# Kernel optimization log

Hardware: AMD Instinct MI355X
Metric: run time of the kernel (lower is better)

Reference implementation:

```python
import jax, jax.numpy as jnp
import numpy as np

# ----- static layer configuration (mirrors __init__ / _precompute_cg_tensor) -----
NODE_LS = [0, 0, 1, 1]          # node_l_values (multiplicity expressed via repetition; node_multiplicity=1)
EDGE_SH = 1                      # edge_sh_degree
H_LS = NODE_LS + NODE_LS + [0]   # l-values of h = [f_src, f_tgt, d]
H_DIMS = [2 * l + 1 for l in H_LS]
H_OFF = np.concatenate([[0], np.cumsum(H_DIMS)])
A_DIMS = [2 * l + 1 for l in range(EDGE_SH + 1)]
A_OFF = np.concatenate([[0], np.cumsum(A_DIMS)])
O_DIMS = [2 * l + 1 for l in NODE_LS]
O_OFF = np.concatenate([[0], np.cumsum(O_DIMS)])
F_DIM = int(O_OFF[-1])           # 8
A_DIM = int(A_OFF[-1])           # 4
N_NODES, N_EDGES = 100000, 1600000
MLP_DIMS = [2 * len(NODE_LS) + 1, 64, 32, len(NODE_LS)]  # 9 -> 64 -> 32 -> 4

def _levi_civita():
    e = np.zeros((3, 3, 3), np.float32)
    e[0, 1, 2] = e[1, 2, 0] = e[2, 0, 1] = 1.0
    e[0, 2, 1] = e[2, 1, 0] = e[1, 0, 2] = -1.0
    return e

# real SO(3) Clebsch-Gordan tensors (e3nn wigner_3j normalization: full contraction norm 1)
_CG = {
    (0, 0, 0): np.ones((1, 1, 1), np.float32),
    (0, 1, 1): (np.eye(3, dtype=np.float32) / np.sqrt(3.0)).reshape(1, 3, 3),
    (1, 0, 1): (np.eye(3, dtype=np.float32) / np.sqrt(3.0)).reshape(3, 1, 3),
    (1, 1, 0): (np.eye(3, dtype=np.float32) / np.sqrt(3.0)).reshape(3, 3, 1),
    (1, 1, 1): _levi_civita() / np.sqrt(6.0),
}

CONNECTIONS = []  # (h_idx, a_l, out_idx, cg[h,a,o]) -- same enumeration order as the torch loop
for _h_idx, _hl in enumerate(H_LS):
    for _al in range(EDGE_SH + 1):
        for _oi, _ol in enumerate(NODE_LS):
            if abs(_hl - _al) <= _ol <= _hl + _al and (_hl, _al, _ol) in _CG:
                CONNECTIONS.append((_h_idx, _al, _oi, jnp.asarray(_CG[(_hl, _al, _ol)])))


def _invariants(x):
    # s_i = [f_{l=0}, ||f_{l=1}||, ...] per l-slot (multiplicity 1)
    outs = []
    for i, l in enumerate(NODE_LS):
        s, e = int(O_OFF[i]), int(O_OFF[i + 1])
        if l == 0:
            outs.append(x[:, s:e])
        else:
            outs.append(jnp.linalg.norm(x[:, s:e], axis=1, keepdims=True))
    return jnp.concatenate(outs, axis=1)


def setup_inputs() -> dict:
    ks = jax.random.split(jax.random.key(0), 10)
    edge_index = jax.random.randint(ks[0], (2, N_EDGES), 0, N_NODES)
    f = jax.random.normal(ks[1], (N_NODES, F_DIM), jnp.float32)
    d = jax.random.uniform(ks[2], (N_EDGES, 1), jnp.float32)
    a = jax.random.normal(ks[3], (N_EDGES, A_DIM), jnp.float32)
    w1 = jax.random.normal(ks[4], (EDGE_SH + 1,), jnp.float32) * 0.1
    w2 = jax.random.normal(ks[5], (EDGE_SH + 1,), jnp.float32) * 0.1
    W0 = jax.random.normal(ks[6], (MLP_DIMS[0], MLP_DIMS[1]), jnp.float32) / np.sqrt(MLP_DIMS[0])
    b0 = jnp.zeros((MLP_DIMS[1],), jnp.float32)
    W1 = jax.random.normal(ks[7], (MLP_DIMS[1], MLP_DIMS[2]), jnp.float32) / np.sqrt(MLP_DIMS[1])
    b1 = jnp.zeros((MLP_DIMS[2],), jnp.float32)
    W2 = jax.random.normal(ks[8], (MLP_DIMS[2], MLP_DIMS[3]), jnp.float32) / np.sqrt(MLP_DIMS[2])
    b2 = jnp.zeros((MLP_DIMS[3],), jnp.float32)
    return {"edge_index": edge_index, "f": f, "d": d, "a": a, "w1": w1, "w2": w2,
            "W0": W0, "b0": b0, "W1": W1, "b1": b1, "W2": W2, "b2": b2}


def reference(edge_index, f, d, a, w1, w2, W0, b0, W1, b1, W2, b2):
    src, tgt = edge_index[0], edge_index[1]
    n = f.shape[0]
    h = jnp.concatenate([f[src], f[tgt], d], axis=1)  # [E, 17]
    messages = jnp.zeros((h.shape[0], F_DIM), f.dtype)
    for h_idx, a_l, out_idx, cg in CONNECTIONS:
        hs, he = int(H_OFF[h_idx]), int(H_OFF[h_idx + 1])
        as_, ae = int(A_OFF[a_l]), int(A_OFF[a_l + 1])
        os_, oe = int(O_OFF[out_idx]), int(O_OFF[out_idx + 1])
        raw = jnp.einsum('hao,eh,ea->eo', cg, h[:, hs:he], a[:, as_:ae])  # [E, 2*out_l+1]
        msg = jnp.tanh(w2[a_l] * jnp.tanh(w1[a_l] * raw))
        messages = messages.at[:, os_:oe].add(msg)
    agg = jax.ops.segment_sum(messages, tgt, num_segments=n)          # [N, 8]
    dist_sum = jax.ops.segment_sum(d, tgt, num_segments=n)           # [N, 1]
    counts = jax.ops.segment_sum(jnp.ones((h.shape[0],), f.dtype), tgt, num_segments=n)
    avg_d = dist_sum / (counts[:, None] + 1e-8)
    psi_in = jnp.concatenate([_invariants(f), _invariants(agg), avg_d], axis=1)  # [N, 9]
    x = jax.nn.relu(psi_in @ W0 + b0)
    x = jax.nn.relu(x @ W1 + b1)
    gates = jax.nn.sigmoid(x @ W2 + b2)  # [N, 4]
    gate_full = jnp.concatenate(
        [jnp.repeat(gates[:, i:i + 1], O_DIMS[i], axis=1) for i in range(len(NODE_LS))], axis=1)
    return f + gate_full * agg
```

## Files before the change

kernel.cpp:

```cpp
#include <hip/hip_runtime.h>
#include <math.h>

#define IS3 0.57735026918962576f
#define IS6 0.40824829046386302f

#define SHIFT 11
#define BSZ   2048
#define CAP   36864u
#define MQ    4096.0f
#define IMQ   (1.0f/4096.0f)

typedef float v2f __attribute__((ext_vector_type(2)));

__device__ __forceinline__ float fastrcp(float x) { return __builtin_amdgcn_rcpf(x); }
__device__ __forceinline__ v2f mk2(float a, float b) { v2f r; r.x = a; r.y = b; return r; }

__device__ __forceinline__ v2f Tnl2(v2f x, v2f tw1, v2f w2) {
    v2f t = tw1 * x;
    v2f e;
    e.x = __expf(t.x);
    e.y = __expf(t.y);
    v2f ep = e + 1.0f;
    v2f r;
    r.x = fastrcp(ep.x);
    r.y = fastrcp(ep.y);
    v2f u = 1.0f - 2.0f * r;
    v2f z = w2 * u;
    v2f z2 = z * z;
    v2f p = z2 * 0.133333333f - 0.333333333f;
    return z * z2 * p + z;
}

__device__ __forceinline__ int q16(float x) {
    int v = (int)rintf(x * MQ);
    v = v >  32767 ?  32767 : v;
    v = v < -32768 ? -32768 : v;
    return v;
}

__global__ __launch_bounds__(256, 8) void route_kernel(
    const int* __restrict__ ei, const float* __restrict__ f,
    const float* __restrict__ d, const float* __restrict__ a,
    const float* __restrict__ w1p, const float* __restrict__ w2p,
    unsigned* __restrict__ tails,
    unsigned* __restrict__ qmeta,
    uint2* __restrict__ qmsg,
    int E, int nbuk)
{
    __shared__ unsigned hcnt[64];
    __shared__ unsigned hoff[64];
    int tid = threadIdx.x;
    if (tid < 64) hcnt[tid] = 0;

    int e = blockIdx.x * 256 + tid;
    bool valid = (e < E);

    float tw10 = 2.0f * w1p[0], tw11 = 2.0f * w1p[1];
    float w20 = w2p[0], w21 = w2p[1];

    int t = 0, s = 0;
    float4 sA = make_float4(0.f,0.f,0.f,0.f), sB = sA, tA = sA, tB = sA, av = sA;
    float de = 0.f;
    if (valid) {
        t = ei[E + e];
        s = ei[e];
        const float4* f4 = (const float4*)f;
        sA = f4[2*s]; sB = f4[2*s+1];
        tA = f4[2*t]; tB = f4[2*t+1];
        de = d[e];
        av = ((const float4*)a)[e];
    }

    __syncthreads();

    unsigned b = 0, lrank = 0;
    if (valid) {
        b = (((unsigned)t) >> SHIFT) & 63u;
        lrank = atomicAdd(&hcnt[b], 1u);
    }
    __syncthreads();

    unsigned basek = 0;
    if (tid < nbuk && hcnt[tid] != 0u)
        basek = atomicAdd(&tails[tid * 64], hcnt[tid]);

    unsigned dq = 0;
    uint2 pk = make_uint2(0u, 0u);
    if (valid) {
        float a0 = av.x, ax = av.y, ay = av.z, az = av.w;
        float axs = ax * IS3, ays = ay * IS3, azs = az * IS3;
        float a03 = a0 * IS3;

        v2f twSX = mk2(tw10, tw11), w2SX = mk2(w20, w21);
        v2f twXY = mk2(tw11, tw11), w2XY = mk2(w21, w21);
        v2f twCX = mk2(tw11, tw10), w2CX = mk2(w21, w20);
        v2f twDD = mk2(tw10, tw10), w2DD = mk2(w20, w20);

        v2f aSX = mk2(a0, axs);
        v2f aYZ = mk2(ays, azs);

        float sc[5] = { sA.x, sA.y, tA.x, tA.y, de };
        float vx[4] = { sA.z, sB.y, tA.z, tB.y };
        float vy[4] = { sA.w, sB.z, tA.w, tB.z };
        float vz[4] = { sB.x, sB.w, tB.x, tB.w };

        v2f mSX = mk2(0.f, 0.f);
        v2f mYZ = mk2(0.f, 0.f);
        float cz6[4];

        #pragma unroll
        for (int i = 0; i < 5; ++i) {
            mSX += Tnl2(sc[i] * aSX, twSX, w2SX);
            mYZ += Tnl2(sc[i] * aYZ, twXY, w2XY);
        }
        #pragma unroll
        for (int i = 0; i < 4; ++i) {
            float dva = vx[i]*ax + vy[i]*ay + vz[i]*az;
            mSX += Tnl2(mk2(dva * IS3, vx[i] * a03), twCX, w2CX);
            mYZ += Tnl2(mk2(vy[i] * a03, vz[i] * a03), twDD, w2DD);
            float cx = vy[i]*az - vz[i]*ay;
            float cy = vz[i]*ax - vx[i]*az;
            float cz = vx[i]*ay - vy[i]*ax;
            v2f exy = Tnl2(mk2(cx * IS6, cy * IS6), twXY, w2XY);
            mSX.y += exy.x;
            mYZ.x += exy.y;
            cz6[i] = cz * IS6;
        }
        v2f g1 = Tnl2(mk2(cz6[0], cz6[1]), twXY, w2XY);
        v2f g2 = Tnl2(mk2(cz6[2], cz6[3]), twXY, w2XY);
        mYZ.y += (g1.x + g1.y) + (g2.x + g2.y);

        unsigned dqi = (unsigned)(de * 2047.0f + 0.5f);
        dq = dqi > 2047u ? 2047u : dqi;
        int qS = q16(mSX.x), qX = q16(mSX.y), qY = q16(mYZ.x), qZ = q16(mYZ.y);
        pk.x = ((unsigned)(unsigned short)qS) | (((unsigned)(unsigned short)qX) << 16);
        pk.y = ((unsigned)(unsigned short)qY) | (((unsigned)(unsigned short)qZ) << 16);
    }

    if (tid < nbuk) hoff[tid] = basek;
    __syncthreads();

    if (valid) {
        unsigned pos = hoff[b] + lrank;
        if (pos < CAP) {
            size_t idx = (size_t)b * CAP + pos;
            qmeta[idx] = (((unsigned)(t & (BSZ - 1))) << 11) | dq;
            qmsg[idx]  = pk;
        }
    }
}

__global__ __launch_bounds__(1024) void bucket_kernel(
    const unsigned* __restrict__ tails, const unsigned* __restrict__ qmeta,
    const uint2* __restrict__ qmsg, unsigned* __restrict__ partial,
    int nbuk, int seg)
{
    __shared__ unsigned long long accSX[BSZ];
    __shared__ unsigned long long accYZ[BSZ];
    __shared__ unsigned accM[BSZ];
    int wg = blockIdx.x;
    int b = wg / seg, sgi = wg % seg;
    for (int i = threadIdx.x; i < BSZ; i += 1024) {
        accSX[i] = 0ull; accYZ[i] = 0ull; accM[i] = 0u;
    }
    __syncthreads();

    unsigned tail = tails[b * 64];
    if (tail > CAP) tail = CAP;
    unsigned lo = (unsigned)(((unsigned long long)tail * sgi) / seg);
    unsigned hi = (unsigned)(((unsigned long long)tail * (sgi + 1)) / seg);
    size_t base = (size_t)b * CAP;

    for (unsigned q = lo + threadIdx.x; q < hi; q += 1024) {
        unsigned meta = qmeta[base + q];
        uint2 m = qmsg[base + q];
        int local = (int)(meta >> 11);
        int qS = (int)(short)(m.x & 0xFFFFu);
        int qX = (int)(short)(m.x >> 16);
        int qY = (int)(short)(m.y & 0xFFFFu);
        int qZ = (int)(short)(m.y >> 16);
        unsigned long long vSX =
            (((unsigned long long)(unsigned)qX) << 32) | (unsigned)(qS + 65536);
        unsigned long long vYZ =
            (((unsigned long long)(unsigned)qZ) << 32) | (unsigned)(qY + 65536);
        atomicAdd(&accSX[local], vSX);
        atomicAdd(&accYZ[local], vYZ);
        atomicAdd(&accM[local], (1u << 20) | (meta & 2047u));
    }
    __syncthreads();

    unsigned* dst = partial + (size_t)wg * (BSZ * 5);
    for (int i = threadIdx.x; i < BSZ; i += 1024) {
        unsigned long long sx = accSX[i], yz = accYZ[i];
        dst[0*BSZ + i] = (unsigned)sx;
        dst[1*BSZ + i] = (unsigned)(sx >> 32);
        dst[2*BSZ + i] = (unsigned)yz;
        dst[3*BSZ + i] = (unsigned)(yz >> 32);
        dst[4*BSZ + i] = accM[i];
    }
}

template<int SEGC>
__global__ __launch_bounds__(128) void mlp_kernel(
    const float* __restrict__ f, const unsigned* __restrict__ partial,
    const float* __restrict__ W0, const float* __restrict__ b0,
    const float* __restrict__ W1, const float* __restrict__ b1,
    const float* __restrict__ W2, const float* __restrict__ b2,
    float* __restrict__ out, int N)
{
    __shared__ float4 sW0t4[64*3];
    __shared__ float4 sW1v[64*8];
    __shared__ float4 sW2v[32];
    __shared__ float  sb0[64];
    __shared__ float4 sb1v[8];
    __shared__ float4 sb2v[1];

    int tid = threadIdx.x;
    int n = blockIdx.x * 128 + tid;
    bool vn = (n < N);
    int nc = vn ? n : (N - 1);

    int b = nc >> SHIFT;
    int local = nc & (BSZ - 1);
    unsigned pl[SEGC][5];
    #pragma unroll
    for (int s2 = 0; s2 < SEGC; ++s2) {
        const unsigned* p = partial + ((size_t)(b * SEGC + s2)) * (BSZ * 5);
        pl[s2][0] = p[0*BSZ + local];
        pl[s2][1] = p[1*BSZ + local];
        pl[s2][2] = p[2*BSZ + local];
        pl[s2][3] = p[3*BSZ + local];
        pl[s2][4] = p[4*BSZ + local];
    }
    float4 fA = ((const float4*)f)[2*nc];
    float4 fB = ((const float4*)f)[2*nc+1];

    float* w0t = (float*)sW0t4;
    for (int idx = tid; idx < 576; idx += 128) {
        int k = idx >> 6, i = idx & 63;
        w0t[i * 12 + k] = W0[idx];
    }
    for (int idx = tid; idx < 192; idx += 128) {
        int i = idx / 3, k = 9 + idx % 3;
        w0t[i * 12 + k] = 0.f;
    }
    { float* p = (float*)sW1v; for (int idx = tid; idx < 2048; idx += 128) p[idx] = W1[idx]; }
    { float* p = (float*)sW2v; if (tid < 128) p[tid] = W2[tid]; }
    if (tid < 64) sb0[tid] = b0[tid];
    { float* p = (float*)sb1v; if (tid < 32) p[tid] = b1[tid]; }
    { float* p = (float*)sb2v; if (tid < 4)  p[tid] = b2[tid]; }
    __syncthreads();

    int S = 0, X = 0, Y = 0, Z = 0, cnt = 0, dqs = 0;
    #pragma unroll
    for (int s2 = 0; s2 < SEGC; ++s2) {
        unsigned m4 = pl[s2][4];
        int c = (int)(m4 >> 20);
        S += (int)pl[s2][0] - (c << 16);
        X += (int)pl[s2][1];
        Y += (int)pl[s2][2] - (c << 16);
        Z += (int)pl[s2][3];
        dqs += (int)(m4 & 0xFFFFFu);
        cnt += c;
    }
    float aS = (float)S * IMQ, ax = (float)X * IMQ;
    float ay = (float)Y * IMQ, az = (float)Z * IMQ;
    float cf = (float)cnt;
    float dsum = (float)dqs * (1.0f / 2047.0f);

    float nrm1 = sqrtf(fA.z*fA.z + fA.w*fA.w + fB.x*fB.x);
    float nrm2 = sqrtf(fB.y*fB.y + fB.z*fB.z + fB.w*fB.w);
    float nv   = sqrtf(ax*ax + ay*ay + az*az);
    float avgd = dsum * fastrcp(cf + 1e-8f);
    float4 p0 = make_float4(fA.x, fA.y, nrm1, nrm2);
    float4 p1 = make_float4(aS, aS, nv, nv);
    float4 p2 = make_float4(avgd, 0.f, 0.f, 0.f);

    float x1s[32];
    #pragma unroll
    for (int j = 0; j < 8; ++j) {
        float4 bv = sb1v[j];
        x1s[4*j+0] = bv.x; x1s[4*j+1] = bv.y; x1s[4*j+2] = bv.z; x1s[4*j+3] = bv.w;
    }
    #pragma unroll
    for (int i = 0; i < 64; ++i) {
        float4 r0 = sW0t4[i*3+0], r1 = sW0t4[i*3+1], r2 = sW0t4[i*3+2];
        float acc = sb0[i]
            + r0.x*p0.x + r0.y*p0.y + r0.z*p0.z + r0.w*p0.w
            + r1.x*p1.x + r1.y*p1.y + r1.z*p1.z + r1.w*p1.w
            + r2.x*p2.x;
        acc = fmaxf(acc, 0.f);
        #pragma unroll
        for (int j = 0; j < 8; ++j) {
            float4 wv = sW1v[i*8+j];
            x1s[4*j+0] += acc * wv.x;
            x1s[4*j+1] += acc * wv.y;
            x1s[4*j+2] += acc * wv.z;
            x1s[4*j+3] += acc * wv.w;
        }
    }
    #pragma unroll
    for (int j = 0; j < 32; ++j) x1s[j] = fmaxf(x1s[j], 0.f);

    float4 gb = sb2v[0];
    float g0 = gb.x, g1 = gb.y, g2 = gb.z, g3 = gb.w;
    #pragma unroll
    for (int i = 0; i < 32; ++i) {
        float4 wv = sW2v[i];
        g0 += x1s[i] * wv.x;
        g1 += x1s[i] * wv.y;
        g2 += x1s[i] * wv.z;
        g3 += x1s[i] * wv.w;
    }
    if (!vn) return;
    g0 = fastrcp(1.0f + __expf(-g0));
    g1 = fastrcp(1.0f + __expf(-g1));
    g2 = fastrcp(1.0f + __expf(-g2));
    g3 = fastrcp(1.0f + __expf(-g3));

    float* o = out + (size_t)8*n;
    o[0] = fA.x + g0*aS;
    o[1] = fA.y + g1*aS;
    o[2] = fA.z + g2*ax;
    o[3] = fA.w + g2*ay;
    o[4] = fB.x + g2*az;
    o[5] = fB.y + g3*ax;
    o[6] = fB.z + g3*ay;
    o[7] = fB.w + g3*az;
}

__global__ __launch_bounds__(128) void mlp_kernel_gen(
    const float* __restrict__ f, const unsigned* __restrict__ partial,
    const float* __restrict__ W0, const float* __restrict__ b0,
    const float* __restrict__ W1, const float* __restrict__ b1,
    const float* __restrict__ W2, const float* __restrict__ b2,
    float* __restrict__ out, int N, int seg)
{
    int n = blockIdx.x * 128 + threadIdx.x;
    if (n >= N) return;

    int b = n >> SHIFT;
    int local = n & (BSZ - 1);
    int S = 0, X = 0, Y = 0, Z = 0, cnt = 0, dqs = 0;
    for (int s2 = 0; s2 < seg; ++s2) {
        const unsigned* p = partial + ((size_t)(b * seg + s2)) * (BSZ * 5);
        unsigned m4 = p[4*BSZ + local];
        int c = (int)(m4 >> 20);
        S += (int)p[0*BSZ + local] - (c << 16);
        X += (int)p[1*BSZ + local];
        Y += (int)p[2*BSZ + local] - (c << 16);
        Z += (int)p[3*BSZ + local];
        dqs += (int)(m4 & 0xFFFFFu);
        cnt += c;
    }
    float aS = (float)S * IMQ, ax = (float)X * IMQ;
    float ay = (float)Y * IMQ, az = (float)Z * IMQ;
    float dsum = (float)dqs * (1.0f / 2047.0f);

    float4 fA = ((const float4*)f)[2*n];
    float4 fB = ((const float4*)f)[2*n+1];

    float nrm1 = sqrtf(fA.z*fA.z + fA.w*fA.w + fB.x*fB.x);
    float nrm2 = sqrtf(fB.y*fB.y + fB.z*fB.z + fB.w*fB.w);
    float nv   = sqrtf(ax*ax + ay*ay + az*az);
    float avgd = dsum * fastrcp((float)cnt + 1e-8f);
    float pk9[9] = { fA.x, fA.y, nrm1, nrm2, aS, aS, nv, nv, avgd };

    float x1s[32];
    #pragma unroll
    for (int j = 0; j < 32; ++j) x1s[j] = b1[j];
    for (int i = 0; i < 64; ++i) {
        float acc = b0[i];
        #pragma unroll
        for (int k = 0; k < 9; ++k) acc += pk9[k] * W0[k*64 + i];
        acc = fmaxf(acc, 0.f);
        #pragma unroll
        for (int j = 0; j < 32; ++j) x1s[j] += acc * W1[i*32 + j];
    }
    #pragma unroll
    for (int j = 0; j < 32; ++j) x1s[j] = fmaxf(x1s[j], 0.f);

    float g0 = b2[0], g1 = b2[1], g2 = b2[2], g3 = b2[3];
    #pragma unroll
    for (int i = 0; i < 32; ++i) {
        g0 += x1s[i] * W2[i*4+0];
        g1 += x1s[i] * W2[i*4+1];
        g2 += x1s[i] * W2[i*4+2];
        g3 += x1s[i] * W2[i*4+3];
    }
    g0 = fastrcp(1.0f + __expf(-g0));
    g1 = fastrcp(1.0f + __expf(-g1));
    g2 = fastrcp(1.0f + __expf(-g2));
    g3 = fastrcp(1.0f + __expf(-g3));

    float* o = out + (size_t)8*n;
    o[0] = fA.x + g0*aS;
    o[1] = fA.y + g1*aS;
    o[2] = fA.z + g2*ax;
    o[3] = fA.w + g2*ay;
    o[4] = fB.x + g2*az;
    o[5] = fB.y + g3*ax;
    o[6] = fB.z + g3*ay;
    o[7] = fB.w + g3*az;
}

extern "C" void kernel_launch(void* const* d_in, const int* in_sizes, int n_in,
                              void* d_out, int out_size, void* d_ws, size_t ws_size,
                              hipStream_t stream) {
    const int*   ei = (const int*)d_in[0];
    const float* f  = (const float*)d_in[1];
    const float* d  = (const float*)d_in[2];
    const float* a  = (const float*)d_in[3];
    const float* w1 = (const float*)d_in[4];
    const float* w2 = (const float*)d_in[5];
    const float* W0 = (const float*)d_in[6];
    const float* b0 = (const float*)d_in[7];
    const float* W1 = (const float*)d_in[8];
    const float* b1 = (const float*)d_in[9];
    const float* W2 = (const float*)d_in[10];
    const float* b2 = (const float*)d_in[11];
    int E = in_sizes[0] / 2;
    int N = in_sizes[1] / 8;
    int nbuk = (N + BSZ - 1) >> SHIFT;

    size_t qn = (size_t)nbuk * CAP;
    size_t fixed = qn * 12 + (size_t)nbuk * 64 * 4;
    size_t per_seg = (size_t)nbuk * BSZ * 5 * 4;
    int segmax = nbuk > 0 ? (512 / nbuk) : 6;
    if (segmax < 1) segmax = 1;
    int seg = 6;
    if (ws_size > fixed + per_seg) {
        size_t m = (ws_size - fixed) / per_seg;
        seg = (int)(m < (size_t)segmax ? m : (size_t)segmax);
        if (seg < 1) seg = 1;
    }

    char* w = (char*)d_ws;
    uint2*    qmsg    = (uint2*)w;
    unsigned* qmeta   = (unsigned*)(w + qn * 8);
    unsigned* partial = (unsigned*)(w + qn * 12);
    unsigned* tails   = (unsigned*)(w + qn * 12 + (size_t)seg * per_seg);

    hipMemsetAsync(tails, 0, (size_t)nbuk * 64 * sizeof(unsigned), stream);

    int EB = (E + 255) / 256;
    route_kernel <<<dim3(EB), dim3(256), 0, stream>>>(
        ei, f, d, a, w1, w2, tails, qmeta, qmsg, E, nbuk);
    bucket_kernel<<<dim3(nbuk * seg), dim3(1024), 0, stream>>>(
        tails, qmeta, qmsg, partial, nbuk, seg);

    dim3 mg((N + 127) / 128), mb(128);
    switch (seg) {
      case 1:  mlp_kernel<1> <<<mg, mb, 0, stream>>>(f, partial, W0,b0,W1,b1,W2,b2, (float*)d_out, N); break;
      case 2:  mlp_kernel<2> <<<mg, mb, 0, stream>>>(f, partial, W0,b0,W1,b1,W2,b2, (float*)d_out, N); break;
      case 3:  mlp_kernel<3> <<<mg, mb, 0, stream>>>(f, partial, W0,b0,W1,b1,W2,b2, (float*)d_out, N); break;
      case 4:  mlp_kernel<4> <<<mg, mb, 0, stream>>>(f, partial, W0,b0,W1,b1,W2,b2, (float*)d_out, N); break;
      case 5:  mlp_kernel<5> <<<mg, mb, 0, stream>>>(f, partial, W0,b0,W1,b1,W2,b2, (float*)d_out, N); break;
      case 6:  mlp_kernel<6> <<<mg, mb, 0, stream>>>(f, partial, W0,b0,W1,b1,W2,b2, (float*)d_out, N); break;
      case 7:  mlp_kernel<7> <<<mg, mb, 0, stream>>>(f, partial, W0,b0,W1,b1,W2,b2, (float*)d_out, N); break;
      case 8:  mlp_kernel<8> <<<mg, mb, 0, stream>>>(f, partial, W0,b0,W1,b1,W2,b2, (float*)d_out, N); break;
      case 9:  mlp_kernel<9> <<<mg, mb, 0, stream>>>(f, partial, W0,b0,W1,b1,W2,b2, (float*)d_out, N); break;
      case 10: mlp_kernel<10><<<mg, mb, 0, stream>>>(f, partial, W0,b0,W1,b1,W2,b2, (float*)d_out, N); break;
      default:
        mlp_kernel_gen<<<mg, mb, 0, stream>>>(f, partial, W0,b0,W1,b1,W2,b2, (float*)d_out, N, seg);
    }
}
```

Measured before the change: 209.5 us.

## Read MLP weights from global memory and enlarge route and MLP blocks

The MLP kernel no longer stages W0/W1/W2 and biases into shared memory. It reads them straight from global memory as uniform float4 loads, and the first layer is restructured into 8-wide hidden tiles. This removes the per-block staging loop and its barrier. Block size also grows from 128 to 256 in the MLP and from 256 to 1024 in the route kernel. That changes per-block histogram granularity in route, and 1024-thread blocks with an occupancy hint of 8 may cut registers or occupancy.

```diff
diff --git a/kernel.cpp b/kernel.cpp
--- a/kernel.cpp
+++ b/kernel.cpp
@@ -38,7 +38,7 @@
     return v;
 }
 
-__global__ __launch_bounds__(256, 8) void route_kernel(
+__global__ __launch_bounds__(1024, 8) void route_kernel(
     const int* __restrict__ ei, const float* __restrict__ f,
     const float* __restrict__ d, const float* __restrict__ a,
     const float* __restrict__ w1p, const float* __restrict__ w2p,
@@ -52,7 +52,7 @@
     int tid = threadIdx.x;
     if (tid < 64) hcnt[tid] = 0;
 
-    int e = blockIdx.x * 256 + tid;
+    int e = blockIdx.x * 1024 + tid;
     bool valid = (e < E);
 
     float tw10 = 2.0f * w1p[0], tw11 = 2.0f * w1p[1];
@@ -201,22 +201,15 @@
 }
 
 template<int SEGC>
-__global__ __launch_bounds__(128) void mlp_kernel(
+__global__ __launch_bounds__(256, 8) void mlp_kernel(
     const float* __restrict__ f, const unsigned* __restrict__ partial,
     const float* __restrict__ W0, const float* __restrict__ b0,
     const float* __restrict__ W1, const float* __restrict__ b1,
     const float* __restrict__ W2, const float* __restrict__ b2,
     float* __restrict__ out, int N)
 {
-    __shared__ float4 sW0t4[64*3];
-    __shared__ float4 sW1v[64*8];
-    __shared__ float4 sW2v[32];
-    __shared__ float  sb0[64];
-    __shared__ float4 sb1v[8];
-    __shared__ float4 sb2v[1];
-
     int tid = threadIdx.x;
-    int n = blockIdx.x * 128 + tid;
+    int n = blockIdx.x * 256 + tid;
     bool vn = (n < N);
     int nc = vn ? n : (N - 1);
 
@@ -234,22 +227,6 @@
     }
     float4 fA = ((const float4*)f)[2*nc];
     float4 fB = ((const float4*)f)[2*nc+1];
-
-    float* w0t = (float*)sW0t4;
-    for (int idx = tid; idx < 576; idx += 128) {
-        int k = idx >> 6, i = idx & 63;
-        w0t[i * 12 + k] = W0[idx];
-    }
-    for (int idx = tid; idx < 192; idx += 128) {
-        int i = idx / 3, k = 9 + idx % 3;
-        w0t[i * 12 + k] = 0.f;
-    }
-    { float* p = (float*)sW1v; for (int idx = tid; idx < 2048; idx += 128) p[idx] = W1[idx]; }
-    { float* p = (float*)sW2v; if (tid < 128) p[tid] = W2[tid]; }
-    if (tid < 64) sb0[tid] = b0[tid];
-    { float* p = (float*)sb1v; if (tid < 32) p[tid] = b1[tid]; }
-    { float* p = (float*)sb2v; if (tid < 4)  p[tid] = b2[tid]; }
-    __syncthreads();
 
     int S = 0, X = 0, Y = 0, Z = 0, cnt = 0, dqs = 0;
     #pragma unroll
@@ -272,41 +249,60 @@
     float nrm2 = sqrtf(fB.y*fB.y + fB.z*fB.z + fB.w*fB.w);
     float nv   = sqrtf(ax*ax + ay*ay + az*az);
     float avgd = dsum * fastrcp(cf + 1e-8f);
-    float4 p0 = make_float4(fA.x, fA.y, nrm1, nrm2);
-    float4 p1 = make_float4(aS, aS, nv, nv);
-    float4 p2 = make_float4(avgd, 0.f, 0.f, 0.f);
+    float pk9[9] = { fA.x, fA.y, nrm1, nrm2, aS, aS, nv, nv, avgd };
+
+    const float4* W0v = (const float4*)W0;
+    const float4* b0v = (const float4*)b0;
+    const float4* W1v = (const float4*)W1;
+    const float4* b1v = (const float4*)b1;
+    const float4* W2v = (const float4*)W2;
+    const float4* b2v = (const float4*)b2;
 
     float x1s[32];
     #pragma unroll
     for (int j = 0; j < 8; ++j) {
-        float4 bv = sb1v[j];
+        float4 bv = b1v[j];
         x1s[4*j+0] = bv.x; x1s[4*j+1] = bv.y; x1s[4*j+2] = bv.z; x1s[4*j+3] = bv.w;
     }
-    #pragma unroll
-    for (int i = 0; i < 64; ++i) {
-        float4 r0 = sW0t4[i*3+0], r1 = sW0t4[i*3+1], r2 = sW0t4[i*3+2];
-        float acc = sb0[i]
-            + r0.x*p0.x + r0.y*p0.y + r0.z*p0.z + r0.w*p0.w
-            + r1.x*p1.x + r1.y*p1.y + r1.z*p1.z + r1.w*p1.w
-            + r2.x*p2.x;
-        acc = fmaxf(acc, 0.f);
-        #pragma unroll
-        for (int j = 0; j < 8; ++j) {
-            float4 wv = sW1v[i*8+j];
-            x1s[4*j+0] += acc * wv.x;
-            x1s[4*j+1] += acc * wv.y;
-            x1s[4*j+2] += acc * wv.z;
-            x1s[4*j+3] += acc * wv.w;
+
+    #pragma unroll
+    for (int tile = 0; tile < 8; ++tile) {
+        float h[8];
+        {
+            float4 ba = b0v[2*tile], bb = b0v[2*tile+1];
+            h[0]=ba.x; h[1]=ba.y; h[2]=ba.z; h[3]=ba.w;
+            h[4]=bb.x; h[5]=bb.y; h[6]=bb.z; h[7]=bb.w;
+        }
+        #pragma unroll
+        for (int k = 0; k < 9; ++k) {
+            float4 wa = W0v[k*16 + 2*tile];
+            float4 wb = W0v[k*16 + 2*tile + 1];
+            float pv = pk9[k];
+            h[0] += pv*wa.x; h[1] += pv*wa.y; h[2] += pv*wa.z; h[3] += pv*wa.w;
+            h[4] += pv*wb.x; h[5] += pv*wb.y; h[6] += pv*wb.z; h[7] += pv*wb.w;
+        }
+        #pragma unroll
+        for (int u = 0; u < 8; ++u) {
+            float acc = fmaxf(h[u], 0.f);
+            int i = 8*tile + u;
+            #pragma unroll
+            for (int j = 0; j < 8; ++j) {
+                float4 wv = W1v[i*8+j];
+                x1s[4*j+0] += acc * wv.x;
+                x1s[4*j+1] += acc * wv.y;
+                x1s[4*j+2] += acc * wv.z;
+                x1s[4*j+3] += acc * wv.w;
+            }
         }
     }
     #pragma unroll
     for (int j = 0; j < 32; ++j) x1s[j] = fmaxf(x1s[j], 0.f);
 
-    float4 gb = sb2v[0];
+    float4 gb = b2v[0];
     float g0 = gb.x, g1 = gb.y, g2 = gb.z, g3 = gb.w;
     #pragma unroll
     for (int i = 0; i < 32; ++i) {
-        float4 wv = sW2v[i];
+        float4 wv = W2v[i];
         g0 += x1s[i] * wv.x;
         g1 += x1s[i] * wv.y;
         g2 += x1s[i] * wv.z;
@@ -329,14 +325,14 @@
     o[7] = fB.w + g3*az;
 }
 
-__global__ __launch_bounds__(128) void mlp_kernel_gen(
+__global__ __launch_bounds__(256) void mlp_kernel_gen(
     const float* __restrict__ f, const unsigned* __restrict__ partial,
     const float* __restrict__ W0, const float* __restrict__ b0,
     const float* __restrict__ W1, const float* __restrict__ b1,
     const float* __restrict__ W2, const float* __restrict__ b2,
     float* __restrict__ out, int N, int seg)
 {
-    int n = blockIdx.x * 128 + threadIdx.x;
+    int n = blockIdx.x * 256 + threadIdx.x;
     if (n >= N) return;
 
     int b = n >> SHIFT;
@@ -443,13 +439,13 @@
 
     hipMemsetAsync(tails, 0, (size_t)nbuk * 64 * sizeof(unsigned), stream);
 
-    int EB = (E + 255) / 256;
-    route_kernel <<<dim3(EB), dim3(256), 0, stream>>>(
+    int EB = (E + 1023) / 1024;
+    route_kernel <<<dim3(EB), dim3(1024), 0, stream>>>(
         ei, f, d, a, w1, w2, tails, qmeta, qmsg, E, nbuk);
     bucket_kernel<<<dim3(nbuk * seg), dim3(1024), 0, stream>>>(
         tails, qmeta, qmsg, partial, nbuk, seg);
 
-    dim3 mg((N + 127) / 128), mb(128);
+    dim3 mg((N + 255) / 256), mb(256);
     switch (seg) {
       case 1:  mlp_kernel<1> <<<mg, mb, 0, stream>>>(f, partial, W0,b0,W1,b1,W2,b2, (float*)d_out, N); break;
       case 2:  mlp_kernel<2> <<<mg, mb, 0, stream>>>(f, partial, W0,b0,W1,b1,W2,b2, (float*)d_out, N); break;
```

Measured after the change: 208.5 us. About the same (-0.5%).
